# Performance work log

Hardware: AMD Instinct MI355X
Metric: run time of the kernel (lower is better)

## Reference

```python
import jax, jax.numpy as jnp
import numpy as np

B, S, H = 64, 512, 768      # batch, subtokens, BERT hidden
N, E = 128, 1024            # word-nodes per graph, directed edges per graph
GH, FH, L = 128, 256, 2     # gnn_hidden, fc_hidden, num_labels


def setup_inputs() -> dict:
    key = jax.random.key(0)
    ks = jax.random.split(key, 14)
    p = lambda k, shp: 0.02 * jax.random.normal(k, shp, jnp.float32)
    return {
        "last_hidden": jax.random.normal(ks[0], (B, S, H), jnp.float32),
        "submap": jax.random.randint(ks[1], (B, S), 0, N, dtype=jnp.int32),
        "edge_index": jax.random.randint(ks[2], (B, 2, E), 0, N, dtype=jnp.int32),
        "num_nodes": N,
        "wr": p(ks[3], (H,)), "br": jnp.zeros((), jnp.float32),
        "W1": p(ks[4], (H, GH)), "b1": jnp.zeros((GH,), jnp.float32),
        "W2": p(ks[5], (GH, GH)), "b2": jnp.zeros((GH,), jnp.float32),
        "Wf1": p(ks[6], (H + GH, FH)), "bf1": jnp.zeros((FH,), jnp.float32),
        "Wf2": p(ks[7], (FH, L)), "bf2": jnp.zeros((L,), jnp.float32),
    }


def reference(last_hidden, submap, edge_index, num_nodes,
              wr, br, W1, b1, W2, b2, Wf1, bf1, Wf2, bf2):
    Bn, Sn, Hn = last_hidden.shape
    Nn = num_nodes
    BN = Bn * Nn

    # --- per-token rationale gating ---
    gate = jax.nn.sigmoid(jnp.einsum("bsh,h->bs", last_hidden, wr) + br)  # [B,S]
    gated = last_hidden * gate[..., None]                                  # [B,S,H]

    # --- subtoken -> word-node mean pooling (batched segment mean) ---
    offs = (jnp.arange(Bn, dtype=submap.dtype) * Nn)[:, None]
    seg = (submap + offs).reshape(-1)                     # [B*S] global node ids
    flat = gated.reshape(Bn * Sn, Hn)
    sums = jax.ops.segment_sum(flat, seg, num_segments=BN)
    cnts = jax.ops.segment_sum(jnp.ones((Bn * Sn,), flat.dtype), seg, num_segments=BN)
    node_feats = sums / jnp.maximum(cnts, 1.0)[:, None]   # zeros where no subtoken maps

    # --- batched GCN message passing (self-loops + PyG gcn_norm) ---
    eoffs = (jnp.arange(Bn, dtype=edge_index.dtype) * Nn)[:, None]
    src = (edge_index[:, 0, :] + eoffs).reshape(-1)       # [B*E]
    dst = (edge_index[:, 1, :] + eoffs).reshape(-1)
    self_idx = jnp.arange(BN, dtype=src.dtype)
    src_all = jnp.concatenate([src, self_idx])
    dst_all = jnp.concatenate([dst, self_idx])
    deg = jax.ops.segment_sum(jnp.ones_like(src_all, jnp.float32), dst_all, num_segments=BN)
    dinv = jax.lax.rsqrt(deg)                             # deg >= 1 due to self-loops
    norm = dinv[src_all] * dinv[dst_all]                  # [B*E + B*N]

    def gcn_layer(x, W, b):
        h = x @ W                                         # transform first (PyG GCNConv)
        msg = h[src_all] * norm[:, None]
        out = jax.ops.segment_sum(msg, dst_all, num_segments=BN) + b
        return jax.nn.relu(out)                           # relu applied in forward()

    x = gcn_layer(node_feats, W1, b1)
    x = gcn_layer(x, W2, b2)

    # --- graph mean pool, concat with CLS, classifier head (dropout = eval identity) ---
    pooled = x.reshape(Bn, Nn, -1).mean(axis=1)           # [B,GH]
    cls_emb = last_hidden[:, 0, :]                        # [B,H]
    h = jax.nn.relu(jnp.concatenate([cls_emb, pooled], axis=1) @ Wf1 + bf1)
    return h @ Wf2 + bf2                                  # [B,num_labels]
```

## Files before the change

### kernel.cpp

```cpp
#include <hip/hip_runtime.h>
#include <math.h>

#define Bz 64
#define Sz 512
#define Hz 768
#define Nz 128
#define Ez 1024
#define GHz 128
#define FHz 256
#define Lz 2
#define BNz (Bz * Nz)

typedef short bf16x8 __attribute__((ext_vector_type(8)));
typedef float f32x4  __attribute__((ext_vector_type(4)));
typedef unsigned short ushort;

__device__ inline ushort f2b(float f) {
    union { float f; unsigned u; } v; v.f = f;
    return (ushort)((v.u + 0x7FFFu + ((v.u >> 16) & 1u)) >> 16);
}

__global__ void k_prep(const float* __restrict__ W1, const float* __restrict__ W2,
                       const int* __restrict__ ei,
                       ushort* __restrict__ W1T, ushort* __restrict__ W2T,
                       int* __restrict__ rowptrG, int* __restrict__ srcsG,
                       float* __restrict__ wnG, float* __restrict__ dinvG) {
    int blk = blockIdx.x, t = threadIdx.x;
    if (blk < 448) {
        int i = blk * 256 + t;
        if (i < Hz * GHz) { int k = i >> 7, n = i & 127; W1T[n * Hz + k] = f2b(W1[i]); }
        int j = i - Hz * GHz;
        if (j >= 0 && j < GHz * GHz) { int k = j >> 7, n = j & 127; W2T[n * GHz + k] = f2b(W2[j]); }
        return;
    }
    int b = blk - 448;
    __shared__ int srcl[Ez], dstl[Ez];
    __shared__ int hist[Nz], off[Nz], rp[Nz + 1];
    __shared__ float di[Nz];
    if (t < Nz) { hist[t] = 0; off[t] = 0; }
    __syncthreads();
    #pragma unroll
    for (int j = 0; j < 4; ++j) {
        int e = t + 256 * j;
        int s = ei[b * 2 * Ez + e], d = ei[b * 2 * Ez + Ez + e];
        srcl[e] = s; dstl[e] = d;
        atomicAdd(&hist[d], 1);
    }
    __syncthreads();
    if (t < Nz) {
        di[t] = rsqrtf((float)hist[t] + 1.0f);
        dinvG[b * Nz + t] = di[t];
    }
    __syncthreads();
    if (t == 0) {
        int run = 0;
        for (int n = 0; n < Nz; ++n) { rp[n] = run; run += hist[n]; }
        rp[Nz] = run;
    }
    __syncthreads();
    #pragma unroll
    for (int j = 0; j < 4; ++j) {
        int e = t + 256 * j;
        int s = srcl[e], d = dstl[e];
        int pos = rp[d] + atomicAdd(&off[d], 1);
        srcsG[b * Ez + pos] = s;
        wnG[b * Ez + pos] = di[s] * di[d];
    }
    if (t < Nz + 1) rowptrG[b * (Nz + 1) + t] = rp[t];
}

__global__ void k_node_gather(const float* __restrict__ lh, const int* __restrict__ submap,
                              const float* __restrict__ wr, const float* __restrict__ br,
                              ushort* __restrict__ nfb) {
    int n = blockIdx.x, b = blockIdx.y;
    int t = threadIdx.x;
    int lane = t & 63, wid = t >> 6;
    __shared__ int list[Sz];
    __shared__ int lcnt;
    __shared__ float partial[Hz];
    if (t == 0) lcnt = 0;
    __syncthreads();
    #pragma unroll
    for (int j = 0; j < 4; ++j) {
        int s = t + 128 * j;
        if (submap[b * Sz + s] == n) { int p = atomicAdd(&lcnt, 1); list[p] = s; }
    }
    __syncthreads();
    int cnt = lcnt;
    float brv = br[0];
    const float* wp = wr + lane * 12;
    float4 w0 = *(const float4*)&wp[0];
    float4 w1 = *(const float4*)&wp[4];
    float4 w2 = *(const float4*)&wp[8];
    float4 a0 = {0,0,0,0}, a1 = {0,0,0,0}, a2 = {0,0,0,0};
    for (int i = wid; i < cnt; i += 2) {
        const float* x = lh + (size_t)(b * Sz + list[i]) * Hz + lane * 12;
        float4 v0 = *(const float4*)&x[0];
        float4 v1 = *(const float4*)&x[4];
        float4 v2 = *(const float4*)&x[8];
        float p = v0.x*w0.x + v0.y*w0.y + v0.z*w0.z + v0.w*w0.w
                + v1.x*w1.x + v1.y*w1.y + v1.z*w1.z + v1.w*w1.w
                + v2.x*w2.x + v2.y*w2.y + v2.z*w2.z + v2.w*w2.w;
        #pragma unroll
        for (int off = 32; off > 0; off >>= 1) p += __shfl_down(p, off);
        float z = __shfl(p, 0) + brv;
        float g = 1.0f / (1.0f + __expf(-z));
        a0.x += g*v0.x; a0.y += g*v0.y; a0.z += g*v0.z; a0.w += g*v0.w;
        a1.x += g*v1.x; a1.y += g*v1.y; a1.z += g*v1.z; a1.w += g*v1.w;
        a2.x += g*v2.x; a2.y += g*v2.y; a2.z += g*v2.z; a2.w += g*v2.w;
    }
    if (wid == 1) {
        float* pp = partial + lane * 12;
        *(float4*)&pp[0] = a0; *(float4*)&pp[4] = a1; *(float4*)&pp[8] = a2;
    }
    __syncthreads();
    if (wid == 0) {
        float invc = 1.0f / fmaxf((float)cnt, 1.0f);
        const float* pp = partial + lane * 12;
        float4 p0 = *(const float4*)&pp[0];
        float4 p1 = *(const float4*)&pp[4];
        float4 p2 = *(const float4*)&pp[8];
        float o[12];
        o[0]=(a0.x+p0.x)*invc; o[1]=(a0.y+p0.y)*invc; o[2]=(a0.z+p0.z)*invc; o[3]=(a0.w+p0.w)*invc;
        o[4]=(a1.x+p1.x)*invc; o[5]=(a1.y+p1.y)*invc; o[6]=(a1.z+p1.z)*invc; o[7]=(a1.w+p1.w)*invc;
        o[8]=(a2.x+p2.x)*invc; o[9]=(a2.y+p2.y)*invc; o[10]=(a2.z+p2.z)*invc; o[11]=(a2.w+p2.w)*invc;
        unsigned* ob = (unsigned*)(nfb + (size_t)(b * Nz + n) * Hz + lane * 12);
        #pragma unroll
        for (int j = 0; j < 6; ++j)
            ob[j] = (unsigned)f2b(o[2*j]) | ((unsigned)f2b(o[2*j+1]) << 16);
    }
}

#define GSP 72
#define HP  132
#define XP  136
__global__ __launch_bounds__(512) void k_gnn_fused(
        const ushort* __restrict__ nfb, const ushort* __restrict__ W1T,
        const ushort* __restrict__ W2T,
        const int* __restrict__ rowptrG, const int* __restrict__ srcsG,
        const float* __restrict__ wnG, const float* __restrict__ dinvG,
        const float* __restrict__ b1, const float* __restrict__ b2,
        const float* __restrict__ lh,
        const float* __restrict__ Wf1, const float* __restrict__ bf1,
        const float* __restrict__ Wf2, const float* __restrict__ bf2,
        float* __restrict__ outG) {
    __shared__ __align__(16) ushort As[128 * GSP];
    __shared__ __align__(16) ushort Bs[128 * GSP];
    __shared__ __align__(16) float  hL[128 * HP];
    __shared__ __align__(16) ushort xb[128 * XP];
    __shared__ int   rp[Nz + 1];
    __shared__ int   srcl[Ez];
    __shared__ float wnl[Ez];
    __shared__ float dil[Nz];
    __shared__ float wsum[8 * 128];

    int b = blockIdx.x;
    int t = threadIdx.x;
    int w = t >> 6, lane = t & 63;
    int q = lane >> 4, l16 = lane & 15;
    int wm = w >> 2, wn2 = w & 3;

    if (t < Nz + 1) rp[t] = rowptrG[b * (Nz + 1) + t];
    if (t < Nz) dil[t] = dinvG[b * Nz + t];
    #pragma unroll
    for (int j = 0; j < 2; ++j) {
        int e = t + 512 * j;
        srcl[e] = srcsG[b * Ez + e];
        wnl[e]  = wnG[b * Ez + e];
    }

    int r0 = t >> 3, s0 = t & 7;
    int r1 = r0 + 64;

    f32x4 acc[4][2];
    #pragma unroll
    for (int mf = 0; mf < 4; ++mf)
        #pragma unroll
        for (int nf = 0; nf < 2; ++nf) acc[mf][nf] = (f32x4){0, 0, 0, 0};

    const ushort* Ab = nfb + (size_t)b * Nz * Hz;
    uint4 apre[2], bpre[2];
    auto loadT1 = [&](int k0) {
        apre[0] = *(const uint4*)&Ab[(size_t)r0 * Hz + k0 + s0 * 8];
        apre[1] = *(const uint4*)&Ab[(size_t)r1 * Hz + k0 + s0 * 8];
        bpre[0] = *(const uint4*)&W1T[(size_t)r0 * Hz + k0 + s0 * 8];
        bpre[1] = *(const uint4*)&W1T[(size_t)r1 * Hz + k0 + s0 * 8];
    };
    loadT1(0);
    for (int k0 = 0; k0 < Hz; k0 += 64) {
        __syncthreads();
        *(uint4*)&As[r0 * GSP + s0 * 8] = apre[0];
        *(uint4*)&As[r1 * GSP + s0 * 8] = apre[1];
        *(uint4*)&Bs[r0 * GSP + s0 * 8] = bpre[0];
        *(uint4*)&Bs[r1 * GSP + s0 * 8] = bpre[1];
        if (k0 + 64 < Hz) loadT1(k0 + 64);
        __syncthreads();
        #pragma unroll
        for (int ks = 0; ks < 64; ks += 32)
            #pragma unroll
            for (int mf = 0; mf < 4; ++mf) {
                bf16x8 af = *(const bf16x8*)&As[(wm * 64 + mf * 16 + l16) * GSP + ks + q * 8];
                #pragma unroll
                for (int nf = 0; nf < 2; ++nf) {
                    bf16x8 bv = *(const bf16x8*)&Bs[(wn2 * 32 + nf * 16 + l16) * GSP + ks + q * 8];
                    acc[mf][nf] = __builtin_amdgcn_mfma_f32_16x16x32_bf16(af, bv, acc[mf][nf], 0, 0, 0);
                }
            }
    }
    #pragma unroll
    for (int mf = 0; mf < 4; ++mf)
        #pragma unroll
        for (int nf = 0; nf < 2; ++nf)
            #pragma unroll
            for (int r = 0; r < 4; ++r)
                hL[(wm * 64 + mf * 16 + q * 4 + r) * HP + wn2 * 32 + nf * 16 + l16] = acc[mf][nf][r];
    __syncthreads();

    float* inL = (float*)As;
    if (t < 256) {
        inL[t]       = lh[(size_t)b * Sz * Hz + t];
        inL[t + 256] = lh[(size_t)b * Sz * Hz + t + 256];
        inL[t + 512] = lh[(size_t)b * Sz * Hz + t + 512];
    }

    float b1v0 = b1[lane], b1v1 = b1[lane + 64];
    for (int d = w; d < Nz; d += 8) {
        float dd = dil[d];
        float a0 = hL[d * HP + lane] * dd * dd;
        float a1 = hL[d * HP + lane + 64] * dd * dd;
        float c0 = 0.f, c1 = 0.f;
        int i = rp[d], pe = rp[d + 1];
        for (; i + 4 <= pe; i += 4) {
            int s0_ = srcl[i], s1_ = srcl[i+1], s2_ = srcl[i+2], s3_ = srcl[i+3];
            float n0 = wnl[i], n1 = wnl[i+1], n2 = wnl[i+2], n3 = wnl[i+3];
            float h0a = hL[s0_*HP+lane], h0b = hL[s0_*HP+lane+64];
            float h1a = hL[s1_*HP+lane], h1b = hL[s1_*HP+lane+64];
            float h2a = hL[s2_*HP+lane], h2b = hL[s2_*HP+lane+64];
            float h3a = hL[s3_*HP+lane], h3b = hL[s3_*HP+lane+64];
            a0 += h0a*n0; a1 += h0b*n0; c0 += h1a*n1; c1 += h1b*n1;
            a0 += h2a*n2; a1 += h2b*n2; c0 += h3a*n3; c1 += h3b*n3;
        }
        for (; i < pe; ++i) {
            int s_ = srcl[i]; float nm = wnl[i];
            a0 += hL[s_*HP+lane]*nm; a1 += hL[s_*HP+lane+64]*nm;
        }
        a0 += c0; a1 += c1;
        xb[d * XP + lane]      = f2b(fmaxf(a0 + b1v0, 0.0f));
        xb[d * XP + lane + 64] = f2b(fmaxf(a1 + b1v1, 0.0f));
    }
    __syncthreads();

    #pragma unroll
    for (int mf = 0; mf < 4; ++mf)
        #pragma unroll
        for (int nf = 0; nf < 2; ++nf) acc[mf][nf] = (f32x4){0, 0, 0, 0};
    for (int k0 = 0; k0 < GHz; k0 += 64) {
        __syncthreads();
        *(uint4*)&Bs[r0 * GSP + s0 * 8] = *(const uint4*)&W2T[(size_t)r0 * GHz + k0 + s0 * 8];
        *(uint4*)&Bs[r1 * GSP + s0 * 8] = *(const uint4*)&W2T[(size_t)r1 * GHz + k0 + s0 * 8];
        __syncthreads();
        #pragma unroll
        for (int ks = 0; ks < 64; ks += 32)
            #pragma unroll
            for (int mf = 0; mf < 4; ++mf) {
                bf16x8 af = *(const bf16x8*)&xb[(wm * 64 + mf * 16 + l16) * XP + k0 + ks + q * 8];
                #pragma unroll
                for (int nf = 0; nf < 2; ++nf) {
                    bf16x8 bv = *(const bf16x8*)&Bs[(wn2 * 32 + nf * 16 + l16) * GSP + ks + q * 8];
                    acc[mf][nf] = __builtin_amdgcn_mfma_f32_16x16x32_bf16(af, bv, acc[mf][nf], 0, 0, 0);
                }
            }
    }
    #pragma unroll
    for (int mf = 0; mf < 4; ++mf)
        #pragma unroll
        for (int nf = 0; nf < 2; ++nf)
            #pragma unroll
            for (int r = 0; r < 4; ++r)
                hL[(wm * 64 + mf * 16 + q * 4 + r) * HP + wn2 * 32 + nf * 16 + l16] = acc[mf][nf][r];
    __syncthreads();

    float b2v0 = b2[lane], b2v1 = b2[lane + 64];
    float p0 = 0.0f, p1 = 0.0f;
    for (int d = w; d < Nz; d += 8) {
        float dd = dil[d];
        float a0 = hL[d * HP + lane] * dd * dd;
        float a1 = hL[d * HP + lane + 64] * dd * dd;
        float c0 = 0.f, c1 = 0.f;
        int i = rp[d], pe = rp[d + 1];
        for (; i + 4 <= pe; i += 4) {
            int s0_ = srcl[i], s1_ = srcl[i+1], s2_ = srcl[i+2], s3_ = srcl[i+3];
            float n0 = wnl[i], n1 = wnl[i+1], n2 = wnl[i+2], n3 = wnl[i+3];
            float h0a = hL[s0_*HP+lane], h0b = hL[s0_*HP+lane+64];
            float h1a = hL[s1_*HP+lane], h1b = hL[s1_*HP+lane+64];
            float h2a = hL[s2_*HP+lane], h2b = hL[s2_*HP+lane+64];
            float h3a = hL[s3_*HP+lane], h3b = hL[s3_*HP+lane+64];
            a0 += h0a*n0; a1 += h0b*n0; c0 += h1a*n1; c1 += h1b*n1;
            a0 += h2a*n2; a1 += h2b*n2; c0 += h3a*n3; c1 += h3b*n3;
        }
        for (; i < pe; ++i) {
            int s_ = srcl[i]; float nm = wnl[i];
            a0 += hL[s_*HP+lane]*nm; a1 += hL[s_*HP+lane+64]*nm;
        }
        a0 += c0; a1 += c1;
        p0 += fmaxf(a0 + b2v0, 0.0f);
        p1 += fmaxf(a1 + b2v1, 0.0f);
    }
    wsum[w * 128 + lane]      = p0;
    wsum[w * 128 + lane + 64] = p1;
    __syncthreads();
    if (t < Nz) {
        float s = 0.0f;
        #pragma unroll
        for (int ww = 0; ww < 8; ++ww) s += wsum[ww * 128 + t];
        inL[Hz + t] = s * (1.0f / Nz);
    }
    __syncthreads();

    float* redW  = (float*)Bs;
    float* hvecL = ((float*)Bs) + 1024;
    {
        int f2 = t & 127, kc4 = t >> 7;
        const float* Wp = Wf1 + (size_t)(kc4 * 224) * FHz + f2 * 2;
        const float* ip = inL + kc4 * 224;
        float ax = 0.f, ay = 0.f;
        #pragma unroll 8
        for (int k = 0; k < 224; ++k) {
            float iv = ip[k];
            float2 wv = *(const float2*)&Wp[(size_t)k * FHz];
            ax += iv * wv.x; ay += iv * wv.y;
        }
        redW[kc4 * 256 + f2 * 2]     = ax;
        redW[kc4 * 256 + f2 * 2 + 1] = ay;
    }
    __syncthreads();
    if (t < 128) {
        float2 s0 = *(const float2*)&redW[t*2],       s1 = *(const float2*)&redW[256 + t*2];
        float2 s2 = *(const float2*)&redW[512 + t*2], s3 = *(const float2*)&redW[768 + t*2];
        float2 bb = *(const float2*)&bf1[t*2];
        hvecL[t*2]     = fmaxf(s0.x + s1.x + s2.x + s3.x + bb.x, 0.0f);
        hvecL[t*2 + 1] = fmaxf(s0.y + s1.y + s2.y + s3.y + bb.y, 0.0f);
    }
    __syncthreads();
    if (t < 128) {
        int l = t >> 6, j0 = t & 63;
        float s = 0.0f;
        #pragma unroll
        for (int m = 0; m < 4; ++m) s += hvecL[j0 + 64*m] * Wf2[(j0 + 64*m) * Lz + l];
        #pragma unroll
        for (int off = 32; off > 0; off >>= 1) s += __shfl_down(s, off);
        if (j0 == 0) outG[b * Lz + l] = s + bf2[l];
    }
}

extern "C" void kernel_launch(void* const* d_in, const int* in_sizes, int n_in,
                              void* d_out, int out_size, void* d_ws, size_t ws_size,
                              hipStream_t stream) {
    const float* lh     = (const float*)d_in[0];
    const int*   submap = (const int*)d_in[1];
    const int*   ei     = (const int*)d_in[2];
    const float* wr  = (const float*)d_in[4];
    const float* br  = (const float*)d_in[5];
    const float* W1  = (const float*)d_in[6];
    const float* b1  = (const float*)d_in[7];
    const float* W2  = (const float*)d_in[8];
    const float* b2  = (const float*)d_in[9];
    const float* Wf1 = (const float*)d_in[10];
    const float* bf1 = (const float*)d_in[11];
    const float* Wf2 = (const float*)d_in[12];
    const float* bf2 = (const float*)d_in[13];
    float* out = (float*)d_out;

    char* p = (char*)d_ws;
    ushort* nfb  = (ushort*)p;  p += (size_t)BNz * Hz * 2;
    ushort* W1T  = (ushort*)p;  p += (size_t)Hz * GHz * 2;
    ushort* W2T  = (ushort*)p;  p += (size_t)GHz * GHz * 2;
    int*    rowptrG = (int*)p;  p += (size_t)Bz * (Nz + 1) * 4;
    int*    srcsG   = (int*)p;  p += (size_t)Bz * Ez * 4;
    float*  wnG     = (float*)p; p += (size_t)Bz * Ez * 4;
    float*  dinvG   = (float*)p; p += (size_t)Bz * Nz * 4;

    k_prep<<<512, 256, 0, stream>>>(W1, W2, ei, W1T, W2T, rowptrG, srcsG, wnG, dinvG);
    k_node_gather<<<dim3(Nz, Bz), 128, 0, stream>>>(lh, submap, wr, br, nfb);
    k_gnn_fused<<<Bz, 512, 0, stream>>>(nfb, W1T, W2T, rowptrG, srcsG, wnG, dinvG,
                                        b1, b2, lh, Wf1, bf1, Wf2, bf2, out);
}
```

Before: 248.0 us.

## Merge prep and gather kernels; widen GNN block to overlap classifier GEMV

```diff
diff --git a/kernel.cpp b/kernel.cpp
--- a/kernel.cpp
+++ b/kernel.cpp
@@ -20,64 +20,73 @@
     return (ushort)((v.u + 0x7FFFu + ((v.u >> 16) & 1u)) >> 16);
 }
 
-__global__ void k_prep(const float* __restrict__ W1, const float* __restrict__ W2,
-                       const int* __restrict__ ei,
-                       ushort* __restrict__ W1T, ushort* __restrict__ W2T,
-                       int* __restrict__ rowptrG, int* __restrict__ srcsG,
-                       float* __restrict__ wnG, float* __restrict__ dinvG) {
+__global__ __launch_bounds__(128) void k_stage(
+        const float* __restrict__ lh, const int* __restrict__ submap,
+        const float* __restrict__ wr, const float* __restrict__ br,
+        const float* __restrict__ W1, const float* __restrict__ W2,
+        const int* __restrict__ ei,
+        ushort* __restrict__ nfb, ushort* __restrict__ W1T, ushort* __restrict__ W2T,
+        int* __restrict__ rowptrG, int* __restrict__ srcsG,
+        float* __restrict__ wnG, float* __restrict__ dinvG) {
     int blk = blockIdx.x, t = threadIdx.x;
-    if (blk < 448) {
-        int i = blk * 256 + t;
-        if (i < Hz * GHz) { int k = i >> 7, n = i & 127; W1T[n * Hz + k] = f2b(W1[i]); }
-        int j = i - Hz * GHz;
-        if (j >= 0 && j < GHz * GHz) { int k = j >> 7, n = j & 127; W2T[n * GHz + k] = f2b(W2[j]); }
-        return;
-    }
-    int b = blk - 448;
-    __shared__ int srcl[Ez], dstl[Ez];
-    __shared__ int hist[Nz], off[Nz], rp[Nz + 1];
-    __shared__ float di[Nz];
-    if (t < Nz) { hist[t] = 0; off[t] = 0; }
-    __syncthreads();
-    #pragma unroll
-    for (int j = 0; j < 4; ++j) {
-        int e = t + 256 * j;
-        int s = ei[b * 2 * Ez + e], d = ei[b * 2 * Ez + Ez + e];
-        srcl[e] = s; dstl[e] = d;
-        atomicAdd(&hist[d], 1);
-    }
-    __syncthreads();
-    if (t < Nz) {
-        di[t] = rsqrtf((float)hist[t] + 1.0f);
-        dinvG[b * Nz + t] = di[t];
-    }
-    __syncthreads();
-    if (t == 0) {
-        int run = 0;
-        for (int n = 0; n < Nz; ++n) { rp[n] = run; run += hist[n]; }
-        rp[Nz] = run;
-    }
-    __syncthreads();
-    #pragma unroll
-    for (int j = 0; j < 4; ++j) {
-        int e = t + 256 * j;
-        int s = srcl[e], d = dstl[e];
-        int pos = rp[d] + atomicAdd(&off[d], 1);
-        srcsG[b * Ez + pos] = s;
-        wnG[b * Ez + pos] = di[s] * di[d];
-    }
-    if (t < Nz + 1) rowptrG[b * (Nz + 1) + t] = rp[t];
-}
-
-__global__ void k_node_gather(const float* __restrict__ lh, const int* __restrict__ submap,
-                              const float* __restrict__ wr, const float* __restrict__ br,
-                              ushort* __restrict__ nfb) {
-    int n = blockIdx.x, b = blockIdx.y;
-    int t = threadIdx.x;
-    int lane = t & 63, wid = t >> 6;
     __shared__ int list[Sz];
     __shared__ int lcnt;
     __shared__ float partial[Hz];
+    __shared__ int srcl2[Ez], dstl2[Ez];
+    __shared__ int hist[Nz], off[Nz], rp[Nz + 1];
+    __shared__ float di[Nz];
+
+    if (blk >= 8192 && blk < 8960) {
+        int i = (blk - 8192) * 128 + t;
+        { int k = i >> 7, n = i & 127; W1T[n * Hz + k] = f2b(W1[i]); }
+        if (i < GHz * GHz) { int k = i >> 7, n = i & 127; W2T[n * GHz + k] = f2b(W2[i]); }
+        return;
+    }
+    if (blk >= 8960) {
+        int b = blk - 8960;
+        if (t < Nz) { hist[t] = 0; off[t] = 0; }
+        __syncthreads();
+        #pragma unroll
+        for (int j = 0; j < 8; ++j) {
+            int e = t + 128 * j;
+            int s = ei[b * 2 * Ez + e], d = ei[b * 2 * Ez + Ez + e];
+            srcl2[e] = s; dstl2[e] = d;
+            atomicAdd(&hist[d], 1);
+        }
+        __syncthreads();
+        if (t < Nz) {
+            di[t] = rsqrtf((float)hist[t] + 1.0f);
+            dinvG[b * Nz + t] = di[t];
+        }
+        __syncthreads();
+        if (t < 64) {
+            int s0 = hist[2 * t], s1 = hist[2 * t + 1];
+            int tot = s0 + s1, run = tot;
+            #pragma unroll
+            for (int o = 1; o < 64; o <<= 1) {
+                int v = __shfl_up(run, o);
+                if (t >= o) run += v;
+            }
+            int excl = run - tot;
+            rp[2 * t] = excl; rp[2 * t + 1] = excl + s0;
+            if (t == 63) rp[Nz] = run;
+        }
+        __syncthreads();
+        #pragma unroll
+        for (int j = 0; j < 8; ++j) {
+            int e = t + 128 * j;
+            int s = srcl2[e], d = dstl2[e];
+            int pos = rp[d] + atomicAdd(&off[d], 1);
+            srcsG[b * Ez + pos] = s;
+            wnG[b * Ez + pos] = di[s] * di[d];
+        }
+        if (t < Nz) rowptrG[b * (Nz + 1) + t] = rp[t];
+        if (t == 0) rowptrG[b * (Nz + 1) + Nz] = rp[Nz];
+        return;
+    }
+
+    int b = blk >> 7, n = blk & 127;
+    int lane = t & 63, wid = t >> 6;
     if (t == 0) lcnt = 0;
     __syncthreads();
     #pragma unroll
@@ -102,7 +111,7 @@
                 + v1.x*w1.x + v1.y*w1.y + v1.z*w1.z + v1.w*w1.w
                 + v2.x*w2.x + v2.y*w2.y + v2.z*w2.z + v2.w*w2.w;
         #pragma unroll
-        for (int off = 32; off > 0; off >>= 1) p += __shfl_down(p, off);
+        for (int o = 32; o > 0; o >>= 1) p += __shfl_down(p, o);
         float z = __shfl(p, 0) + brv;
         float g = 1.0f / (1.0f + __expf(-z));
         a0.x += g*v0.x; a0.y += g*v0.y; a0.z += g*v0.z; a0.w += g*v0.w;
@@ -134,7 +143,7 @@
 #define GSP 72
 #define HP  132
 #define XP  136
-__global__ __launch_bounds__(512) void k_gnn_fused(
+__global__ __launch_bounds__(1024) void k_gnn_fused(
         const ushort* __restrict__ nfb, const ushort* __restrict__ W1T,
         const ushort* __restrict__ W2T,
         const int* __restrict__ rowptrG, const int* __restrict__ srcsG,
@@ -152,7 +161,7 @@
     __shared__ int   srcl[Ez];
     __shared__ float wnl[Ez];
     __shared__ float dil[Nz];
-    __shared__ float wsum[8 * 128];
+    __shared__ float wsum[16 * 128];
 
     int b = blockIdx.x;
     int t = threadIdx.x;
@@ -162,44 +171,35 @@
 
     if (t < Nz + 1) rp[t] = rowptrG[b * (Nz + 1) + t];
     if (t < Nz) dil[t] = dinvG[b * Nz + t];
+    srcl[t] = srcsG[b * Ez + t];
+    wnl[t]  = wnG[b * Ez + t];
+
+    int ar = t >> 3, as_ = t & 7;
+
+    f32x4 acc[2][2];
     #pragma unroll
-    for (int j = 0; j < 2; ++j) {
-        int e = t + 512 * j;
-        srcl[e] = srcsG[b * Ez + e];
-        wnl[e]  = wnG[b * Ez + e];
-    }
-
-    int r0 = t >> 3, s0 = t & 7;
-    int r1 = r0 + 64;
-
-    f32x4 acc[4][2];
-    #pragma unroll
-    for (int mf = 0; mf < 4; ++mf)
+    for (int mf = 0; mf < 2; ++mf)
         #pragma unroll
         for (int nf = 0; nf < 2; ++nf) acc[mf][nf] = (f32x4){0, 0, 0, 0};
 
     const ushort* Ab = nfb + (size_t)b * Nz * Hz;
-    uint4 apre[2], bpre[2];
+    uint4 apre, bpre;
     auto loadT1 = [&](int k0) {
-        apre[0] = *(const uint4*)&Ab[(size_t)r0 * Hz + k0 + s0 * 8];
-        apre[1] = *(const uint4*)&Ab[(size_t)r1 * Hz + k0 + s0 * 8];
-        bpre[0] = *(const uint4*)&W1T[(size_t)r0 * Hz + k0 + s0 * 8];
-        bpre[1] = *(const uint4*)&W1T[(size_t)r1 * Hz + k0 + s0 * 8];
+        apre = *(const uint4*)&Ab[(size_t)ar * Hz + k0 + as_ * 8];
+        bpre = *(const uint4*)&W1T[(size_t)ar * Hz + k0 + as_ * 8];
     };
     loadT1(0);
     for (int k0 = 0; k0 < Hz; k0 += 64) {
         __syncthreads();
-        *(uint4*)&As[r0 * GSP + s0 * 8] = apre[0];
-        *(uint4*)&As[r1 * GSP + s0 * 8] = apre[1];
-        *(uint4*)&Bs[r0 * GSP + s0 * 8] = bpre[0];
-        *(uint4*)&Bs[r1 * GSP + s0 * 8] = bpre[1];
+        *(uint4*)&As[ar * GSP + as_ * 8] = apre;
+        *(uint4*)&Bs[ar * GSP + as_ * 8] = bpre;
         if (k0 + 64 < Hz) loadT1(k0 + 64);
         __syncthreads();
         #pragma unroll
         for (int ks = 0; ks < 64; ks += 32)
             #pragma unroll
-            for (int mf = 0; mf < 4; ++mf) {
-                bf16x8 af = *(const bf16x8*)&As[(wm * 64 + mf * 16 + l16) * GSP + ks + q * 8];
+            for (int mf = 0; mf < 2; ++mf) {
+                bf16x8 af = *(const bf16x8*)&As[(wm * 32 + mf * 16 + l16) * GSP + ks + q * 8];
                 #pragma unroll
                 for (int nf = 0; nf < 2; ++nf) {
                     bf16x8 bv = *(const bf16x8*)&Bs[(wn2 * 32 + nf * 16 + l16) * GSP + ks + q * 8];
@@ -208,23 +208,95 @@
             }
     }
     #pragma unroll
-    for (int mf = 0; mf < 4; ++mf)
+    for (int mf = 0; mf < 2; ++mf)
         #pragma unroll
         for (int nf = 0; nf < 2; ++nf)
             #pragma unroll
             for (int r = 0; r < 4; ++r)
-                hL[(wm * 64 + mf * 16 + q * 4 + r) * HP + wn2 * 32 + nf * 16 + l16] = acc[mf][nf][r];
-    __syncthreads();
-
-    float* inL = (float*)As;
-    if (t < 256) {
-        inL[t]       = lh[(size_t)b * Sz * Hz + t];
-        inL[t + 256] = lh[(size_t)b * Sz * Hz + t + 256];
-        inL[t + 512] = lh[(size_t)b * Sz * Hz + t + 512];
-    }
-
-    float b1v0 = b1[lane], b1v1 = b1[lane + 64];
-    for (int d = w; d < Nz; d += 8) {
+                hL[(wm * 32 + mf * 16 + q * 4 + r) * HP + wn2 * 32 + nf * 16 + l16] = acc[mf][nf][r];
+    __syncthreads();
+
+    float* inL  = (float*)As;
+    float* redA = inL + 896;
+    if (t < 224) ((float4*)inL)[t] = ((const float4*)(lh + (size_t)b * Sz * Hz))[t];
+    __syncthreads();
+
+    if (w < 8) {
+        float b1v0 = b1[lane], b1v1 = b1[lane + 64];
+        for (int d = w; d < Nz; d += 8) {
+            float dd = dil[d];
+            float a0 = hL[d * HP + lane] * dd * dd;
+            float a1 = hL[d * HP + lane + 64] * dd * dd;
+            float c0 = 0.f, c1 = 0.f;
+            int i = rp[d], pe = rp[d + 1];
+            for (; i + 4 <= pe; i += 4) {
+                int s0_ = srcl[i], s1_ = srcl[i+1], s2_ = srcl[i+2], s3_ = srcl[i+3];
+                float n0 = wnl[i], n1 = wnl[i+1], n2 = wnl[i+2], n3 = wnl[i+3];
+                float h0a = hL[s0_*HP+lane], h0b = hL[s0_*HP+lane+64];
+                float h1a = hL[s1_*HP+lane], h1b = hL[s1_*HP+lane+64];
+                float h2a = hL[s2_*HP+lane], h2b = hL[s2_*HP+lane+64];
+                float h3a = hL[s3_*HP+lane], h3b = hL[s3_*HP+lane+64];
+                a0 += h0a*n0; a1 += h0b*n0; c0 += h1a*n1; c1 += h1b*n1;
+                a0 += h2a*n2; a1 += h2b*n2; c0 += h3a*n3; c1 += h3b*n3;
+            }
+            for (; i < pe; ++i) {
+                int s_ = srcl[i]; float nm = wnl[i];
+                a0 += hL[s_*HP+lane]*nm; a1 += hL[s_*HP+lane+64]*nm;
+            }
+            a0 += c0; a1 += c1;
+            xb[d * XP + lane]      = f2b(fmaxf(a0 + b1v0, 0.0f));
+            xb[d * XP + lane + 64] = f2b(fmaxf(a1 + b1v1, 0.0f));
+        }
+    } else {
+        int tt = t - 512;
+        int f2 = tt & 127, kq = tt >> 7;
+        const float* Wp = Wf1 + (size_t)(kq * 192) * FHz + f2 * 2;
+        const float* ip = inL + kq * 192;
+        float ax = 0.f, ay = 0.f;
+        #pragma unroll 8
+        for (int k = 0; k < 192; ++k) {
+            float iv = ip[k];
+            float2 wv = *(const float2*)&Wp[(size_t)k * FHz];
+            ax += iv * wv.x; ay += iv * wv.y;
+        }
+        redA[kq * 256 + f2 * 2]     = ax;
+        redA[kq * 256 + f2 * 2 + 1] = ay;
+    }
+    __syncthreads();
+
+    #pragma unroll
+    for (int mf = 0; mf < 2; ++mf)
+        #pragma unroll
+        for (int nf = 0; nf < 2; ++nf) acc[mf][nf] = (f32x4){0, 0, 0, 0};
+    for (int k0 = 0; k0 < GHz; k0 += 64) {
+        __syncthreads();
+        *(uint4*)&Bs[ar * GSP + as_ * 8] = *(const uint4*)&W2T[(size_t)ar * GHz + k0 + as_ * 8];
+        __syncthreads();
+        #pragma unroll
+        for (int ks = 0; ks < 64; ks += 32)
+            #pragma unroll
+            for (int mf = 0; mf < 2; ++mf) {
+                bf16x8 af = *(const bf16x8*)&xb[(wm * 32 + mf * 16 + l16) * XP + k0 + ks + q * 8];
+                #pragma unroll
+                for (int nf = 0; nf < 2; ++nf) {
+                    bf16x8 bv = *(const bf16x8*)&Bs[(wn2 * 32 + nf * 16 + l16) * GSP + ks + q * 8];
+                    acc[mf][nf] = __builtin_amdgcn_mfma_f32_16x16x32_bf16(af, bv, acc[mf][nf], 0, 0, 0);
+                }
+            }
+    }
+    __syncthreads();
+    #pragma unroll
+    for (int mf = 0; mf < 2; ++mf)
+        #pragma unroll
+        for (int nf = 0; nf < 2; ++nf)
+            #pragma unroll
+            for (int r = 0; r < 4; ++r)
+                hL[(wm * 32 + mf * 16 + q * 4 + r) * HP + wn2 * 32 + nf * 16 + l16] = acc[mf][nf][r];
+    __syncthreads();
+
+    float b2v0 = b2[lane], b2v1 = b2[lane + 64];
+    float p0 = 0.0f, p1 = 0.0f;
+    for (int d = w; d < Nz; d += 16) {
         float dd = dil[d];
         float a0 = hL[d * HP + lane] * dd * dd;
         float a1 = hL[d * HP + lane + 64] * dd * dd;
@@ -245,64 +317,6 @@
             a0 += hL[s_*HP+lane]*nm; a1 += hL[s_*HP+lane+64]*nm;
         }
         a0 += c0; a1 += c1;
-        xb[d * XP + lane]      = f2b(fmaxf(a0 + b1v0, 0.0f));
-        xb[d * XP + lane + 64] = f2b(fmaxf(a1 + b1v1, 0.0f));
-    }
-    __syncthreads();
-
-    #pragma unroll
-    for (int mf = 0; mf < 4; ++mf)
-        #pragma unroll
-        for (int nf = 0; nf < 2; ++nf) acc[mf][nf] = (f32x4){0, 0, 0, 0};
-    for (int k0 = 0; k0 < GHz; k0 += 64) {
-        __syncthreads();
-        *(uint4*)&Bs[r0 * GSP + s0 * 8] = *(const uint4*)&W2T[(size_t)r0 * GHz + k0 + s0 * 8];
-        *(uint4*)&Bs[r1 * GSP + s0 * 8] = *(const uint4*)&W2T[(size_t)r1 * GHz + k0 + s0 * 8];
-        __syncthreads();
-        #pragma unroll
-        for (int ks = 0; ks < 64; ks += 32)
-            #pragma unroll
-            for (int mf = 0; mf < 4; ++mf) {
-                bf16x8 af = *(const bf16x8*)&xb[(wm * 64 + mf * 16 + l16) * XP + k0 + ks + q * 8];
-                #pragma unroll
-                for (int nf = 0; nf < 2; ++nf) {
-                    bf16x8 bv = *(const bf16x8*)&Bs[(wn2 * 32 + nf * 16 + l16) * GSP + ks + q * 8];
-                    acc[mf][nf] = __builtin_amdgcn_mfma_f32_16x16x32_bf16(af, bv, acc[mf][nf], 0, 0, 0);
-                }
-            }
-    }
-    #pragma unroll
-    for (int mf = 0; mf < 4; ++mf)
-        #pragma unroll
-        for (int nf = 0; nf < 2; ++nf)
-            #pragma unroll
-            for (int r = 0; r < 4; ++r)
-                hL[(wm * 64 + mf * 16 + q * 4 + r) * HP + wn2 * 32 + nf * 16 + l16] = acc[mf][nf][r];
-    __syncthreads();
-
-    float b2v0 = b2[lane], b2v1 = b2[lane + 64];
-    float p0 = 0.0f, p1 = 0.0f;
-    for (int d = w; d < Nz; d += 8) {
-        float dd = dil[d];
-        float a0 = hL[d * HP + lane] * dd * dd;
-        float a1 = hL[d * HP + lane + 64] * dd * dd;
-        float c0 = 0.f, c1 = 0.f;
-        int i = rp[d], pe = rp[d + 1];
-        for (; i + 4 <= pe; i += 4) {
-            int s0_ = srcl[i], s1_ = srcl[i+1], s2_ = srcl[i+2], s3_ = srcl[i+3];
-            float n0 = wnl[i], n1 = wnl[i+1], n2 = wnl[i+2], n3 = wnl[i+3];
-            float h0a = hL[s0_*HP+lane], h0b = hL[s0_*HP+lane+64];
-            float h1a = hL[s1_*HP+lane], h1b = hL[s1_*HP+lane+64];
-            float h2a = hL[s2_*HP+lane], h2b = hL[s2_*HP+lane+64];
-            float h3a = hL[s3_*HP+lane], h3b = hL[s3_*HP+lane+64];
-            a0 += h0a*n0; a1 += h0b*n0; c0 += h1a*n1; c1 += h1b*n1;
-            a0 += h2a*n2; a1 += h2b*n2; c0 += h3a*n3; c1 += h3b*n3;
-        }
-        for (; i < pe; ++i) {
-            int s_ = srcl[i]; float nm = wnl[i];
-            a0 += hL[s_*HP+lane]*nm; a1 += hL[s_*HP+lane+64]*nm;
-        }
-        a0 += c0; a1 += c1;
         p0 += fmaxf(a0 + b2v0, 0.0f);
         p1 += fmaxf(a1 + b2v1, 0.0f);
     }
@@ -312,43 +326,45 @@
     if (t < Nz) {
         float s = 0.0f;
         #pragma unroll
-        for (int ww = 0; ww < 8; ++ww) s += wsum[ww * 128 + t];
+        for (int ww = 0; ww < 16; ++ww) s += wsum[ww * 128 + t];
         inL[Hz + t] = s * (1.0f / Nz);
     }
     __syncthreads();
 
-    float* redW  = (float*)Bs;
-    float* hvecL = ((float*)Bs) + 1024;
+    float* redB  = (float*)Bs;
+    float* hvecL = ((float*)Bs) + 2048;
     {
-        int f2 = t & 127, kc4 = t >> 7;
-        const float* Wp = Wf1 + (size_t)(kc4 * 224) * FHz + f2 * 2;
-        const float* ip = inL + kc4 * 224;
+        int f2 = t & 127, kc8 = t >> 7;
+        const float* Wp = Wf1 + (size_t)(Hz + kc8 * 16) * FHz + f2 * 2;
+        const float* ip = inL + Hz + kc8 * 16;
         float ax = 0.f, ay = 0.f;
-        #pragma unroll 8
-        for (int k = 0; k < 224; ++k) {
+        #pragma unroll
+        for (int k = 0; k < 16; ++k) {
             float iv = ip[k];
             float2 wv = *(const float2*)&Wp[(size_t)k * FHz];
             ax += iv * wv.x; ay += iv * wv.y;
         }
-        redW[kc4 * 256 + f2 * 2]     = ax;
-        redW[kc4 * 256 + f2 * 2 + 1] = ay;
+        redB[kc8 * 256 + f2 * 2]     = ax;
+        redB[kc8 * 256 + f2 * 2 + 1] = ay;
     }
     __syncthreads();
     if (t < 128) {
-        float2 s0 = *(const float2*)&redW[t*2],       s1 = *(const float2*)&redW[256 + t*2];
-        float2 s2 = *(const float2*)&redW[512 + t*2], s3 = *(const float2*)&redW[768 + t*2];
-        float2 bb = *(const float2*)&bf1[t*2];
-        hvecL[t*2]     = fmaxf(s0.x + s1.x + s2.x + s3.x + bb.x, 0.0f);
-        hvecL[t*2 + 1] = fmaxf(s0.y + s1.y + s2.y + s3.y + bb.y, 0.0f);
+        float sx = bf1[2 * t], sy = bf1[2 * t + 1];
+        #pragma unroll
+        for (int m = 0; m < 4; ++m) { sx += redA[m * 256 + 2 * t]; sy += redA[m * 256 + 2 * t + 1]; }
+        #pragma unroll
+        for (int m = 0; m < 8; ++m) { sx += redB[m * 256 + 2 * t]; sy += redB[m * 256 + 2 * t + 1]; }
+        hvecL[2 * t]     = fmaxf(sx, 0.0f);
+        hvecL[2 * t + 1] = fmaxf(sy, 0.0f);
     }
     __syncthreads();
     if (t < 128) {
         int l = t >> 6, j0 = t & 63;
         float s = 0.0f;
         #pragma unroll
-        for (int m = 0; m < 4; ++m) s += hvecL[j0 + 64*m] * Wf2[(j0 + 64*m) * Lz + l];
-        #pragma unroll
-        for (int off = 32; off > 0; off >>= 1) s += __shfl_down(s, off);
+        for (int m = 0; m < 4; ++m) s += hvecL[j0 + 64 * m] * Wf2[(j0 + 64 * m) * Lz + l];
+        #pragma unroll
+        for (int o = 32; o > 0; o >>= 1) s += __shfl_down(s, o);
         if (j0 == 0) outG[b * Lz + l] = s + bf2[l];
     }
 }
@@ -380,8 +396,8 @@
     float*  wnG     = (float*)p; p += (size_t)Bz * Ez * 4;
     float*  dinvG   = (float*)p; p += (size_t)Bz * Nz * 4;
 
-    k_prep<<<512, 256, 0, stream>>>(W1, W2, ei, W1T, W2T, rowptrG, srcsG, wnG, dinvG);
-    k_node_gather<<<dim3(Nz, Bz), 128, 0, stream>>>(lh, submap, wr, br, nfb);
-    k_gnn_fused<<<Bz, 512, 0, stream>>>(nfb, W1T, W2T, rowptrG, srcsG, wnG, dinvG,
-                                        b1, b2, lh, Wf1, bf1, Wf2, bf2, out);
+    k_stage<<<8192 + 768 + 64, 128, 0, stream>>>(lh, submap, wr, br, W1, W2, ei,
+                                                 nfb, W1T, W2T, rowptrG, srcsG, wnG, dinvG);
+    k_gnn_fused<<<Bz, 1024, 0, stream>>>(nfb, W1T, W2T, rowptrG, srcsG, wnG, dinvG,
+                                         b1, b2, lh, Wf1, bf1, Wf2, bf2, out);
 }
```

New measurement: 213.9 us. 1.16x faster.
